# Optimization experiments

Measured on AMD Instinct MI355X. Metric: run time of the kernel, lower is better.

The kernel has to match this reference:

```python
import jax, jax.numpy as jnp
import numpy as np

K = 9          # number of umbrella neighbors (excluding self)
BN_EPS = 1e-5


def setup_inputs() -> dict:
    key = jax.random.key(0)
    ks = jax.random.split(key, 8)
    B, N, C = 4, 8192, 3
    ch = 7
    x = jax.random.normal(ks[0], (B, N, C), jnp.float32)
    w1 = jax.random.normal(ks[1], (ch, ch), jnp.float32) * 0.4
    gamma1 = jnp.ones((ch,), jnp.float32)
    beta1 = jnp.zeros((ch,), jnp.float32)
    w2 = jax.random.normal(ks[2], (ch, ch), jnp.float32) * 0.4
    bias2 = jax.random.normal(ks[3], (ch,), jnp.float32) * 0.1
    gamma2 = jnp.ones((ch,), jnp.float32)
    beta2 = jnp.zeros((ch,), jnp.float32)
    w3 = jax.random.normal(ks[4], (ch, ch), jnp.float32) * 0.4
    bias3 = jax.random.normal(ks[5], (ch,), jnp.float32) * 0.1
    return dict(x=x, w1=w1, gamma1=gamma1, beta1=beta1, w2=w2, bias2=bias2,
                gamma2=gamma2, beta2=beta2, w3=w3, bias3=bias3)


def _bn(t, gamma, beta):
    # BatchNorm2d in training mode: batch stats over (B, N, K) per channel (last dim)
    m = t.mean(axis=(0, 1, 2))
    v = t.var(axis=(0, 1, 2))  # biased, matching torch BN normalization
    return (t - m) * jax.lax.rsqrt(v + BN_EPS) * gamma + beta


def reference(x, w1, gamma1, beta1, w2, bias2, gamma2, beta2, w3, bias3):
    B, N, _ = x.shape
    # ---- kNN (negative squared distance, top-k largest == nearest) ----
    xsq = jnp.sum(x * x, axis=-1)                       # [B,N]
    xx = jnp.einsum('bnc,bmc->bnm', x, x)               # [B,N,N]
    dist = 2.0 * xx - xsq[:, :, None] - xsq[:, None, :]
    idx = jax.lax.top_k(dist, K + 1)[1]                 # [B,N,K+1], includes self
    # ---- gather neighbor coords, recenter, drop self ----
    nbr = jax.vmap(lambda xb, ib: xb[ib])(x, idx)       # [B,N,K+1,3]
    nbr = nbr - x[:, :, None, :]
    nbr = nbr[:, :, 1:, :]                              # [B,N,K,3]
    # ---- sort neighbors by azimuth phi ----
    phi = jnp.arctan2(nbr[..., 1], nbr[..., 0]) / (2.0 * np.pi) + 0.5
    order = jnp.argsort(phi, axis=-1)                   # [B,N,K]
    srt = jnp.take_along_axis(nbr, order[..., None], axis=2)  # [B,N,K,3]
    # ---- umbrella pairs: (v_i, v_{i+1 mod K}) ----
    v1 = srt
    v2 = jnp.roll(srt, -1, axis=2)
    centroids = 0.5 * (v1 + v2)                         # [B,N,K,3]
    normals = jnp.cross(v1, v2) + 1e-5
    normals = normals / jnp.linalg.norm(normals, axis=-1, keepdims=True)
    # flip so the first normal's x-component is positive (per point)
    pos_mask = (normals[:, :, 0:1, 0] > 0).astype(x.dtype) * 2.0 - 1.0  # [B,N,1]
    normals = normals * pos_mask[..., None]
    positions = jnp.sum(centroids * normals, axis=-1) / jnp.sqrt(jnp.asarray(3.0, x.dtype))
    feat = jnp.concatenate([centroids, normals, positions[..., None]], axis=-1)  # [B,N,K,7]
    # ---- tiny 1x1 conv MLP (channel-last einsum) + BN + ReLU ----
    h = jnp.einsum('bnkc,oc->bnko', feat, w1)
    h = jax.nn.relu(_bn(h, gamma1, beta1))
    h = jnp.einsum('bnkc,oc->bnko', h, w2) + bias2
    h = jax.nn.relu(_bn(h, gamma2, beta2))
    h = jnp.einsum('bnkc,oc->bnko', h, w3) + bias3
    pooled = jnp.max(h, axis=2)                         # [B,N,7]
    return jnp.concatenate([x, pooled], axis=-1)        # [B,N,10]
```

## Files before the change

kernel.cpp:

```cpp
#include <hip/hip_runtime.h>
#include <math.h>

#define BB 4
#define NN 8192
#define TOTAL (BB*NN)
#define KNBR 9
#define CH 7
#define NCHUNK 16
#define CHUNK (NN/NCHUNK)
#define SLOTS 8
#define NROWS (NCHUNK*SLOTS)
#define GSEL 20
#define QB 4
#define BN_EPS 1e-5f
#define M_ELEMS (TOTAL*KNBR)
#define NREP 64
#define RSTR 32
#define NBLK 256
#define NLEAF 16
#define LSTR 16

#define OFF_PTS   0
#define OFF_PI    524288
#define OFF_STATS 17301504
#define OFF_H1    17317888

__device__ __forceinline__ void ibody(float (&dl)[10], int (&il)[10], float d, int ii) {
    bool c0 = d > dl[0];
#pragma unroll
    for (int p = 9; p > 0; p--) {
        bool here = d > dl[p];
        bool up   = d > dl[p-1];
        float nd = up ? dl[p-1] : d;
        int   ni = up ? il[p-1] : ii;
        if (here) { dl[p] = nd; il[p] = ni; }
    }
    if (c0) { dl[0] = d; il[0] = ii; }
}

__device__ __forceinline__ void insert10(float (&dl)[10], int (&il)[10], float d, int ii) {
    if (d > dl[9]) ibody(dl, il, d, ii);
}

__global__ __launch_bounds__(256) void knn_k(const float* __restrict__ x,
                                             float4* __restrict__ pts,
                                             unsigned int* __restrict__ pi,
                                             float* __restrict__ stats) {
    const int b = blockIdx.z, chunk = blockIdx.y;
    const int c0 = chunk * CHUNK;

    if (blockIdx.x == 0 && blockIdx.y == 0 && blockIdx.z == 0) {
        for (int i = threadIdx.x; i < NREP*RSTR + NLEAF*LSTR + 32; i += 256)
            stats[i] = 0.f;
    }

    __shared__ float4 tile[CHUNK];
    if (threadIdx.x < CHUNK/4) {
        const float4* __restrict__ x4 = (const float4*)(x + (long)(b*NN + c0)*3);
        int t = threadIdx.x;
        float4 f0 = x4[3*t], f1 = x4[3*t+1], f2 = x4[3*t+2];
        float px[4] = {f0.x, f0.w, f1.z, f2.y};
        float py[4] = {f0.y, f1.x, f1.w, f2.z};
        float pz[4] = {f0.z, f1.y, f2.x, f2.w};
#pragma unroll
        for (int u = 0; u < 4; u++) {
            float sq = __fadd_rn(__fadd_rn(__fmul_rn(px[u],px[u]), __fmul_rn(py[u],py[u])),
                                 __fmul_rn(pz[u],pz[u]));
            tile[4*t+u] = make_float4(px[u], py[u], pz[u], sq);
        }
    }
    __syncthreads();

    if (blockIdx.x == 0) {
#pragma unroll
        for (int j = 0; j < CHUNK/256; j++)
            pts[b*NN + c0 + threadIdx.x + j*256] = tile[threadIdx.x + j*256];
    }

    const int q0 = blockIdx.x * (256*QB) + threadIdx.x;
    float qx2[QB], qy2[QB], qz2[QB], nqb[QB];
#pragma unroll
    for (int v = 0; v < QB; v++) {
        long qoff = (long)(b*NN + q0 + v*256) * 3;
        float qx = x[qoff], qy = x[qoff+1], qz = x[qoff+2];
        float qw = qx*qx + qy*qy + qz*qz;
        qx2[v] = qx + qx; qy2[v] = qy + qy; qz2[v] = qz + qz;
        nqb[v] = -1.0f - qw;
    }

    unsigned int m[QB][SLOTS];
#pragma unroll
    for (int v = 0; v < QB; v++)
#pragma unroll
        for (int s = 0; s < SLOTS; s++) m[v][s] = 0xFFFFFFFFu;

#pragma unroll 4
    for (int j = 0; j < CHUNK; j++) {
        float4 t = tile[j];
#pragma unroll
        for (int v = 0; v < QB; v++) {
            float d = fmaf(qx2[v], t.x, fmaf(qy2[v], t.y, fmaf(qz2[v], t.z, nqb[v] - t.w)));
            unsigned int kd = (__float_as_uint(d) & 0xFFFFFE00u) | (unsigned int)j;
#pragma unroll
            for (int p = SLOTS-1; p >= 1; p--)
                asm("v_med3_u32 %0, %1, %2, %3" : "=v"(m[v][p]) : "v"(kd), "v"(m[v][p-1]), "v"(m[v][p]));
            m[v][0] = kd < m[v][0] ? kd : m[v][0];
        }
    }

#pragma unroll
    for (int v = 0; v < QB; v++) {
        int g = b*NN + q0 + v*256;
#pragma unroll
        for (int s = 0; s < SLOTS; s++) {
            unsigned int mm = m[v][s];
            unsigned int key = (mm & 0xFFFFE000u) | (unsigned int)(c0 + (int)(mm & 511u));
            pi[(long)(chunk*SLOTS + s)*TOTAL + g] = key;
        }
    }
}

__global__ __launch_bounds__(128) void geom_k(const float4* __restrict__ pts,
                                              const unsigned int* __restrict__ pi,
                                              const float* __restrict__ w1,
                                              float* __restrict__ h1, float* __restrict__ stats) {
    __shared__ float sw1[49];
    __shared__ float acc[14];
    if (threadIdx.x < 49) sw1[threadIdx.x] = w1[threadIdx.x];
    if (threadIdx.x < 14) acc[threadIdx.x] = 0.f;
    __syncthreads();

    int g = blockIdx.x * 128 + threadIdx.x;
    int b = g >> 13, n = g & (NN-1);
    const float4* __restrict__ base = pts + b*NN;
    float4 qp = base[n];
    float qn = -qp.w;

    unsigned int mk[GSEL];
#pragma unroll
    for (int s = 0; s < GSEL; s++) mk[s] = 0xFFFFFFFFu;
#pragma unroll 1
    for (int e8 = 0; e8 < NROWS/8; e8++) {
        unsigned int pk[8];
#pragma unroll
        for (int u = 0; u < 8; u++) pk[u] = pi[(long)(e8*8 + u)*TOTAL + g];
#pragma unroll
        for (int u = 0; u < 8; u++) {
            unsigned int kd = pk[u];
#pragma unroll
            for (int p = GSEL-1; p >= 1; p--)
                asm("v_med3_u32 %0, %1, %2, %3" : "=v"(mk[p]) : "v"(kd), "v"(mk[p-1]), "v"(mk[p]));
            mk[0] = kd < mk[0] ? kd : mk[0];
        }
    }

    float dl[10]; int il[10];
#pragma unroll
    for (int j = 0; j < 10; j++) { dl[j] = -INFINITY; il[j] = 0; }
#pragma unroll
    for (int hb = 0; hb < 2; hb++) {
        int id[10];
        float4 pp[10];
#pragma unroll
        for (int v = 0; v < 10; v++) { id[v] = (int)(mk[hb*10 + v] & 8191u); pp[v] = base[id[v]]; }
        float dd[10];
#pragma unroll
        for (int v = 0; v < 10; v++) {
            float dot2 = __fadd_rn(__fadd_rn(__fmul_rn(qp.x, 2.f*pp[v].x),
                                             __fmul_rn(qp.y, 2.f*pp[v].y)),
                                   __fmul_rn(qp.z, 2.f*pp[v].z));
            dd[v] = __fsub_rn(__fadd_rn(dot2, qn), pp[v].w);
        }
#pragma unroll
        for (int v = 0; v < 10; v++) insert10(dl, il, dd[v], id[v]);
    }

    float vx[9], vy[9], vz[9], ph[9];
#pragma unroll
    for (int t = 0; t < 9; t++) {
        float4 p4 = base[il[t+1]];
        vx[t] = p4.x - qp.x; vy[t] = p4.y - qp.y; vz[t] = p4.z - qp.z;
        ph[t] = atan2f(vy[t], vx[t]) / 6.283185307179586f + 0.5f;
    }

    int rank[9];
#pragma unroll
    for (int t = 0; t < 9; t++) {
        int r = 0;
#pragma unroll
        for (int u = 0; u < 9; u++) {
            if (u == t) continue;
            bool before = (ph[u] < ph[t]) || (ph[u] == ph[t] && u < t);
            r += before ? 1 : 0;
        }
        rank[t] = r;
    }
    float sx[9], sy[9], sz[9];
#pragma unroll
    for (int s = 0; s < 9; s++) {
        float a = 0.f, bb = 0.f, c = 0.f;
#pragma unroll
        for (int t = 0; t < 9; t++) {
            bool m = (rank[t] == s);
            a = m ? vx[t] : a; bb = m ? vy[t] : bb; c = m ? vz[t] : c;
        }
        sx[s] = a; sy[s] = bb; sz[s] = c;
    }

    float sgn;
    {
        float ax = sx[0], ay = sy[0], az = sz[0];
        float bx = sx[1], by = sy[1], bz = sz[1];
        float nx0 = ay*bz - az*by + 1e-5f;
        float ny0 = az*bx - ax*bz + 1e-5f;
        float nz0 = ax*by - ay*bx + 1e-5f;
        float inv = 1.0f / sqrtf(nx0*nx0 + ny0*ny0 + nz0*nz0);
        sgn = (nx0*inv > 0.0f) ? 1.0f : -1.0f;
    }

    float sum[7], sumsq[7];
#pragma unroll
    for (int o = 0; o < 7; o++) { sum[o] = 0.f; sumsq[o] = 0.f; }

#pragma unroll
    for (int t = 0; t < 9; t++) {
        const int t2 = (t + 1) % 9;
        float ax = sx[t],  ay = sy[t],  az = sz[t];
        float bx = sx[t2], by = sy[t2], bz = sz[t2];
        float cx = 0.5f*(ax+bx), cy = 0.5f*(ay+by), cz = 0.5f*(az+bz);
        float nx0 = ay*bz - az*by + 1e-5f;
        float ny0 = az*bx - ax*bz + 1e-5f;
        float nz0 = ax*by - ay*bx + 1e-5f;
        float inv = 1.0f / sqrtf(nx0*nx0 + ny0*ny0 + nz0*nz0);
        float nx = nx0*inv*sgn, ny = ny0*inv*sgn, nz = nz0*inv*sgn;
        float pos = (cx*nx + cy*ny + cz*nz) / 1.7320508075688772f;

        float f[7] = {cx, cy, cz, nx, ny, nz, pos};
        float* outp = h1 + ((long)g*9 + t) * 7;
#pragma unroll
        for (int o = 0; o < 7; o++) {
            float h = 0.f;
#pragma unroll
            for (int c = 0; c < 7; c++) h += f[c] * sw1[o*7 + c];
            outp[o] = h;
            sum[o] += h; sumsq[o] += h*h;
        }
    }

#pragma unroll
    for (int o = 0; o < 7; o++) {
        float s  = sum[o];
        float s2 = sumsq[o];
        for (int off = 32; off > 0; off >>= 1) { s += __shfl_down(s, off); s2 += __shfl_down(s2, off); }
        if ((threadIdx.x & 63) == 0) {
            atomicAdd(&acc[o], s);
            atomicAdd(&acc[7 + o], s2);
        }
    }
    __syncthreads();
    if (threadIdx.x < 14)
        atomicAdd(&stats[(blockIdx.x & (NREP-1))*RSTR + threadIdx.x], acc[threadIdx.x]);
}

__device__ __forceinline__ void grid_barrier(int* cnt) {
    __syncthreads();
    if (threadIdx.x == 0) {
        __threadfence();
        int* leaf = &cnt[(blockIdx.x & (NLEAF-1)) * LSTR];
        int old = __hip_atomic_fetch_add(leaf, 1, __ATOMIC_ACQ_REL, __HIP_MEMORY_SCOPE_AGENT);
        if (old == (NBLK/NLEAF) - 1) {
            int rold = __hip_atomic_fetch_add(&cnt[NLEAF*LSTR], 1, __ATOMIC_ACQ_REL, __HIP_MEMORY_SCOPE_AGENT);
            if (rold == NLEAF - 1)
                __hip_atomic_store(&cnt[NLEAF*LSTR + 16], 1, __ATOMIC_RELEASE, __HIP_MEMORY_SCOPE_AGENT);
        }
        while (__hip_atomic_load(&cnt[NLEAF*LSTR + 16], __ATOMIC_ACQUIRE, __HIP_MEMORY_SCOPE_AGENT) == 0)
            __builtin_amdgcn_s_sleep(8);
        __threadfence();
    }
    __syncthreads();
}

__global__ __launch_bounds__(128) void tail_k(const float* __restrict__ x,
                                              const float* __restrict__ h1,
                                              const float* __restrict__ gamma1, const float* __restrict__ beta1,
                                              const float* __restrict__ w2, const float* __restrict__ bias2,
                                              const float* __restrict__ gamma2, const float* __restrict__ beta2,
                                              const float* __restrict__ w3, const float* __restrict__ bias3,
                                              float* __restrict__ stats, float* __restrict__ out) {
    __shared__ float sw2[49], sw3[49], sb2[7], sb3[7];
    __shared__ float acc[14];
    __shared__ float sco[14];
    if (threadIdx.x < 49) { sw2[threadIdx.x] = w2[threadIdx.x]; sw3[threadIdx.x] = w3[threadIdx.x]; }
    if (threadIdx.x < 7)  { sb2[threadIdx.x] = bias2[threadIdx.x]; sb3[threadIdx.x] = bias3[threadIdx.x]; }
    if (threadIdx.x < 14) acc[threadIdx.x] = 0.f;

    int* cnt = (int*)(stats + NREP*RSTR);
    int g = blockIdx.x * 128 + threadIdx.x;
    const float invM = 1.0f / (float)M_ELEMS;

    if (threadIdx.x < 7) {
        int c = threadIdx.x;
        float sm = 0.f, sq = 0.f;
#pragma unroll
        for (int r = 0; r < NREP; r++) { sm += stats[r*RSTR + c]; sq += stats[r*RSTR + 7 + c]; }
        float m = sm * invM;
        float v = sq * invM - m*m;
        float sc = gamma1[c] / sqrtf(v + BN_EPS);
        sco[c] = sc; sco[7 + c] = beta1[c] - m*sc;
    }
    __syncthreads();
    float s1v[7], b1v[7];
#pragma unroll
    for (int c = 0; c < 7; c++) { s1v[c] = sco[c]; b1v[c] = sco[7 + c]; }

    float hv[63];
    float sum[7], sumsq[7];
#pragma unroll
    for (int o = 0; o < 7; o++) { sum[o] = 0.f; sumsq[o] = 0.f; }
    const float* hh = h1 + (long)g * 63;
#pragma unroll
    for (int t = 0; t < 9; t++) {
        float a[7];
#pragma unroll
        for (int c = 0; c < 7; c++) a[c] = fmaxf(hh[t*7 + c]*s1v[c] + b1v[c], 0.0f);
#pragma unroll
        for (int o = 0; o < 7; o++) {
            float h = 0.f;
#pragma unroll
            for (int c = 0; c < 7; c++) h += a[c] * sw2[o*7 + c];
            h += sb2[o];
            hv[t*7 + o] = h;
            sum[o] += h; sumsq[o] += h*h;
        }
    }
#pragma unroll
    for (int o = 0; o < 7; o++) {
        float s  = sum[o];
        float s2 = sumsq[o];
        for (int off = 32; off > 0; off >>= 1) { s += __shfl_down(s, off); s2 += __shfl_down(s2, off); }
        if ((threadIdx.x & 63) == 0) {
            atomicAdd(&acc[o], s);
            atomicAdd(&acc[7 + o], s2);
        }
    }
    __syncthreads();
    if (threadIdx.x < 14)
        atomicAdd(&stats[(blockIdx.x & (NREP-1))*RSTR + 14 + threadIdx.x], acc[threadIdx.x]);

    grid_barrier(cnt);

    if (threadIdx.x < 7) {
        int c = threadIdx.x;
        float sm = 0.f, sq = 0.f;
#pragma unroll
        for (int r = 0; r < NREP; r++) {
            sm += __hip_atomic_load(&stats[r*RSTR + 14 + c], __ATOMIC_RELAXED, __HIP_MEMORY_SCOPE_AGENT);
            sq += __hip_atomic_load(&stats[r*RSTR + 21 + c], __ATOMIC_RELAXED, __HIP_MEMORY_SCOPE_AGENT);
        }
        float m = sm * invM;
        float v = sq * invM - m*m;
        float sc = gamma2[c] / sqrtf(v + BN_EPS);
        sco[c] = sc; sco[7 + c] = beta2[c] - m*sc;
    }
    __syncthreads();

    float pooled[7];
#pragma unroll
    for (int o = 0; o < 7; o++) pooled[o] = -INFINITY;
#pragma unroll
    for (int t = 0; t < 9; t++) {
        float a[7];
#pragma unroll
        for (int c = 0; c < 7; c++) a[c] = fmaxf(hv[t*7 + c]*sco[c] + sco[7 + c], 0.0f);
#pragma unroll
        for (int o = 0; o < 7; o++) {
            float h = 0.f;
#pragma unroll
            for (int c = 0; c < 7; c++) h += a[c] * sw3[o*7 + c];
            h += sb3[o];
            pooled[o] = fmaxf(pooled[o], h);
        }
    }
    out[g*10 + 0] = x[g*3 + 0];
    out[g*10 + 1] = x[g*3 + 1];
    out[g*10 + 2] = x[g*3 + 2];
#pragma unroll
    for (int o = 0; o < 7; o++) out[g*10 + 3 + o] = pooled[o];
}

extern "C" void kernel_launch(void* const* d_in, const int* in_sizes, int n_in,
                              void* d_out, int out_size, void* d_ws, size_t ws_size,
                              hipStream_t stream) {
    const float* x      = (const float*)d_in[0];
    const float* w1     = (const float*)d_in[1];
    const float* gamma1 = (const float*)d_in[2];
    const float* beta1  = (const float*)d_in[3];
    const float* w2     = (const float*)d_in[4];
    const float* bias2  = (const float*)d_in[5];
    const float* gamma2 = (const float*)d_in[6];
    const float* beta2  = (const float*)d_in[7];
    const float* w3     = (const float*)d_in[8];
    const float* bias3  = (const float*)d_in[9];
    float* out = (float*)d_out;

    char* ws = (char*)d_ws;
    float4*       pts  = (float4*)(ws + OFF_PTS);
    unsigned int* pi   = (unsigned int*)(ws + OFF_PI);
    float*        stats= (float*)(ws + OFF_STATS);
    float*        h1   = (float*)(ws + OFF_H1);

    knn_k <<<dim3(NN/(256*QB), NCHUNK, BB), 256, 0, stream>>>(x, pts, pi, stats);
    geom_k<<<TOTAL/128, 128, 0, stream>>>(pts, pi, w1, h1, stats);
    tail_k<<<NBLK, 128, 0, stream>>>(x, h1, gamma1, beta1, w2, bias2,
                                     gamma2, beta2, w3, bias3, stats, out);
}
```

Measured before the change: 227.8 us.

## Split geometry kernel into neighbor-select and feature kernels, transpose h1 layout

Splits the former geom_k into sel_k, which merges candidate rows and picks the 10 nearest, writing 9 neighbor indices as ushort, and feat_k, which computes the umbrella features. feat_k stages neighbor offsets in LDS and indexes them through an inverse permutation instead of a register select network. h1 is stored channel-major (coalesced per thread index) instead of per-point interleaved. Exact rescoring is done in five batches of 4 instead of two of 10. The aim is lower register pressure and better coalescing, at the cost of an extra launch and an index round trip through global memory.

Result: slower. 241.5 us (+6.0%).

```diff
diff --git a/kernel.cpp b/kernel.cpp
--- a/kernel.cpp
+++ b/kernel.cpp
@@ -22,8 +22,9 @@
 
 #define OFF_PTS   0
 #define OFF_PI    524288
-#define OFF_STATS 17301504
-#define OFF_H1    17317888
+#define OFF_NBR   17301504
+#define OFF_STATS 17891328
+#define OFF_H1    17901568
 
 __device__ __forceinline__ void ibody(float (&dl)[10], int (&il)[10], float d, int ii) {
     bool c0 = d > dl[0];
@@ -120,16 +121,9 @@
     }
 }
 
-__global__ __launch_bounds__(128) void geom_k(const float4* __restrict__ pts,
-                                              const unsigned int* __restrict__ pi,
-                                              const float* __restrict__ w1,
-                                              float* __restrict__ h1, float* __restrict__ stats) {
-    __shared__ float sw1[49];
-    __shared__ float acc[14];
-    if (threadIdx.x < 49) sw1[threadIdx.x] = w1[threadIdx.x];
-    if (threadIdx.x < 14) acc[threadIdx.x] = 0.f;
-    __syncthreads();
-
+__global__ __launch_bounds__(128) void sel_k(const float4* __restrict__ pts,
+                                             const unsigned int* __restrict__ pi,
+                                             unsigned short* __restrict__ nbr) {
     int g = blockIdx.x * 128 + threadIdx.x;
     int b = g >> 13, n = g & (NN-1);
     const float4* __restrict__ base = pts + b*NN;
@@ -157,30 +151,52 @@
     float dl[10]; int il[10];
 #pragma unroll
     for (int j = 0; j < 10; j++) { dl[j] = -INFINITY; il[j] = 0; }
-#pragma unroll
-    for (int hb = 0; hb < 2; hb++) {
-        int id[10];
-        float4 pp[10];
-#pragma unroll
-        for (int v = 0; v < 10; v++) { id[v] = (int)(mk[hb*10 + v] & 8191u); pp[v] = base[id[v]]; }
-        float dd[10];
-#pragma unroll
-        for (int v = 0; v < 10; v++) {
+#pragma unroll 1
+    for (int hb = 0; hb < 5; hb++) {
+        int id[4]; float4 pp[4]; float dd[4];
+#pragma unroll
+        for (int v = 0; v < 4; v++) { id[v] = (int)(mk[hb*4 + v] & 8191u); pp[v] = base[id[v]]; }
+#pragma unroll
+        for (int v = 0; v < 4; v++) {
             float dot2 = __fadd_rn(__fadd_rn(__fmul_rn(qp.x, 2.f*pp[v].x),
                                              __fmul_rn(qp.y, 2.f*pp[v].y)),
                                    __fmul_rn(qp.z, 2.f*pp[v].z));
             dd[v] = __fsub_rn(__fadd_rn(dot2, qn), pp[v].w);
         }
 #pragma unroll
-        for (int v = 0; v < 10; v++) insert10(dl, il, dd[v], id[v]);
-    }
-
-    float vx[9], vy[9], vz[9], ph[9];
+        for (int v = 0; v < 4; v++) insert10(dl, il, dd[v], id[v]);
+    }
+
+#pragma unroll
+    for (int t = 0; t < 9; t++)
+        nbr[(long)t*TOTAL + g] = (unsigned short)il[t+1];
+}
+
+__global__ __launch_bounds__(128) void feat_k(const float4* __restrict__ pts,
+                                              const unsigned short* __restrict__ nbr,
+                                              const float* __restrict__ w1,
+                                              float* __restrict__ h1, float* __restrict__ stats) {
+    __shared__ float sw1[49];
+    __shared__ float acc[14];
+    __shared__ float vbx[9][128], vby[9][128], vbz[9][128];
+    if (threadIdx.x < 49) sw1[threadIdx.x] = w1[threadIdx.x];
+    if (threadIdx.x < 14) acc[threadIdx.x] = 0.f;
+    __syncthreads();
+
+    int tid = threadIdx.x;
+    int g = blockIdx.x * 128 + tid;
+    int b = g >> 13, n = g & (NN-1);
+    const float4* __restrict__ base = pts + b*NN;
+    float4 qp = base[n];
+
+    float ph[9];
 #pragma unroll
     for (int t = 0; t < 9; t++) {
-        float4 p4 = base[il[t+1]];
-        vx[t] = p4.x - qp.x; vy[t] = p4.y - qp.y; vz[t] = p4.z - qp.z;
-        ph[t] = atan2f(vy[t], vx[t]) / 6.283185307179586f + 0.5f;
+        int idx = (int)nbr[(long)t*TOTAL + g];
+        float4 p4 = base[idx];
+        float vx = p4.x - qp.x, vy = p4.y - qp.y, vz = p4.z - qp.z;
+        vbx[t][tid] = vx; vby[t][tid] = vy; vbz[t][tid] = vz;
+        ph[t] = atan2f(vy, vx) / 6.283185307179586f + 0.5f;
     }
 
     int rank[9];
@@ -195,27 +211,25 @@
         }
         rank[t] = r;
     }
-    float sx[9], sy[9], sz[9];
+    int inv[9];
 #pragma unroll
     for (int s = 0; s < 9; s++) {
-        float a = 0.f, bb = 0.f, c = 0.f;
-#pragma unroll
-        for (int t = 0; t < 9; t++) {
-            bool m = (rank[t] == s);
-            a = m ? vx[t] : a; bb = m ? vy[t] : bb; c = m ? vz[t] : c;
-        }
-        sx[s] = a; sy[s] = bb; sz[s] = c;
+        int sel = 0;
+#pragma unroll
+        for (int t = 0; t < 9; t++) sel = (rank[t] == s) ? t : sel;
+        inv[s] = sel;
     }
 
     float sgn;
     {
-        float ax = sx[0], ay = sy[0], az = sz[0];
-        float bx = sx[1], by = sy[1], bz = sz[1];
+        int t1 = inv[0], t2 = inv[1];
+        float ax = vbx[t1][tid], ay = vby[t1][tid], az = vbz[t1][tid];
+        float bx = vbx[t2][tid], by = vby[t2][tid], bz = vbz[t2][tid];
         float nx0 = ay*bz - az*by + 1e-5f;
         float ny0 = az*bx - ax*bz + 1e-5f;
         float nz0 = ax*by - ay*bx + 1e-5f;
-        float inv = 1.0f / sqrtf(nx0*nx0 + ny0*ny0 + nz0*nz0);
-        sgn = (nx0*inv > 0.0f) ? 1.0f : -1.0f;
+        float inv2 = 1.0f / sqrtf(nx0*nx0 + ny0*ny0 + nz0*nz0);
+        sgn = (nx0*inv2 > 0.0f) ? 1.0f : -1.0f;
     }
 
     float sum[7], sumsq[7];
@@ -223,26 +237,25 @@
     for (int o = 0; o < 7; o++) { sum[o] = 0.f; sumsq[o] = 0.f; }
 
 #pragma unroll
-    for (int t = 0; t < 9; t++) {
-        const int t2 = (t + 1) % 9;
-        float ax = sx[t],  ay = sy[t],  az = sz[t];
-        float bx = sx[t2], by = sy[t2], bz = sz[t2];
+    for (int s = 0; s < 9; s++) {
+        int t1 = inv[s], t2 = inv[(s+1) % 9];
+        float ax = vbx[t1][tid], ay = vby[t1][tid], az = vbz[t1][tid];
+        float bx = vbx[t2][tid], by = vby[t2][tid], bz = vbz[t2][tid];
         float cx = 0.5f*(ax+bx), cy = 0.5f*(ay+by), cz = 0.5f*(az+bz);
         float nx0 = ay*bz - az*by + 1e-5f;
         float ny0 = az*bx - ax*bz + 1e-5f;
         float nz0 = ax*by - ay*bx + 1e-5f;
-        float inv = 1.0f / sqrtf(nx0*nx0 + ny0*ny0 + nz0*nz0);
-        float nx = nx0*inv*sgn, ny = ny0*inv*sgn, nz = nz0*inv*sgn;
+        float inv2 = 1.0f / sqrtf(nx0*nx0 + ny0*ny0 + nz0*nz0);
+        float nx = nx0*inv2*sgn, ny = ny0*inv2*sgn, nz = nz0*inv2*sgn;
         float pos = (cx*nx + cy*ny + cz*nz) / 1.7320508075688772f;
 
         float f[7] = {cx, cy, cz, nx, ny, nz, pos};
-        float* outp = h1 + ((long)g*9 + t) * 7;
 #pragma unroll
         for (int o = 0; o < 7; o++) {
             float h = 0.f;
 #pragma unroll
             for (int c = 0; c < 7; c++) h += f[c] * sw1[o*7 + c];
-            outp[o] = h;
+            h1[(long)(s*7 + o)*TOTAL + g] = h;
             sum[o] += h; sumsq[o] += h*h;
         }
     }
@@ -317,12 +330,12 @@
     float sum[7], sumsq[7];
 #pragma unroll
     for (int o = 0; o < 7; o++) { sum[o] = 0.f; sumsq[o] = 0.f; }
-    const float* hh = h1 + (long)g * 63;
 #pragma unroll
     for (int t = 0; t < 9; t++) {
         float a[7];
 #pragma unroll
-        for (int c = 0; c < 7; c++) a[c] = fmaxf(hh[t*7 + c]*s1v[c] + b1v[c], 0.0f);
+        for (int c = 0; c < 7; c++)
+            a[c] = fmaxf(h1[(long)(t*7 + c)*TOTAL + g]*s1v[c] + b1v[c], 0.0f);
 #pragma unroll
         for (int o = 0; o < 7; o++) {
             float h = 0.f;
@@ -404,13 +417,15 @@
     float* out = (float*)d_out;
 
     char* ws = (char*)d_ws;
-    float4*       pts  = (float4*)(ws + OFF_PTS);
-    unsigned int* pi   = (unsigned int*)(ws + OFF_PI);
-    float*        stats= (float*)(ws + OFF_STATS);
-    float*        h1   = (float*)(ws + OFF_H1);
+    float4*         pts  = (float4*)(ws + OFF_PTS);
+    unsigned int*   pi   = (unsigned int*)(ws + OFF_PI);
+    unsigned short* nbr  = (unsigned short*)(ws + OFF_NBR);
+    float*          stats= (float*)(ws + OFF_STATS);
+    float*          h1   = (float*)(ws + OFF_H1);
 
     knn_k <<<dim3(NN/(256*QB), NCHUNK, BB), 256, 0, stream>>>(x, pts, pi, stats);
-    geom_k<<<TOTAL/128, 128, 0, stream>>>(pts, pi, w1, h1, stats);
+    sel_k <<<TOTAL/128, 128, 0, stream>>>(pts, pi, nbr);
+    feat_k<<<TOTAL/128, 128, 0, stream>>>(pts, nbr, w1, h1, stats);
     tail_k<<<NBLK, 128, 0, stream>>>(x, h1, gamma1, beta1, w2, bias2,
                                      gamma2, beta2, w3, bias3, stats, out);
 }
```
